# Kernel tuning notes

Measured on AMD Instinct MI355X. Metric: run time of the kernel, lower is better.

The kernel has to match this reference:

```python
import jax, jax.numpy as jnp
import numpy as np

B, T, OBS, H, LAT = 512, 512, 64, 256, 16
NEG_SLOPE = 0.01  # flax nn.leaky_relu default


def _glorot(key, shape):
    fan_in, fan_out = shape[0], shape[-1]
    s = jnp.sqrt(6.0 / (fan_in + fan_out))
    return jax.random.uniform(key, shape, jnp.float32, -s, s)


def setup_inputs() -> dict:
    key = jax.random.key(0)
    ks = jax.random.split(key, 12)
    x = jax.random.normal(ks[0], (B, T, OBS), jnp.float32)
    lengths = jax.random.randint(ks[1], (B,), T // 4, T + 1)
    mask = jnp.arange(T)[None, :] < lengths[:, None]  # [B,T] bool, prefix-valid
    return {
        "x": x,
        "mask": mask,
        # encoder params
        "Wip": _glorot(ks[2], (OBS, H)), "bip": jnp.zeros((H,)),
        "Wi_e": _glorot(ks[3], (H, 4 * H)), "Wh_e": _glorot(ks[4], (H, 4 * H)),
        "b_e": jnp.zeros((4 * H,)),
        "Wlp": _glorot(ks[5], (H, LAT)), "blp": jnp.zeros((LAT,)),
        # decoder params
        "Wle": _glorot(ks[6], (LAT, H)), "ble": jnp.zeros((H,)),
        "Wi_d": _glorot(ks[7], (H, 4 * H)), "Wh_d": _glorot(ks[8], (H, 4 * H)),
        "b_d": jnp.zeros((4 * H,)),
        "Wop": _glorot(ks[9], (H, OBS)), "bop": jnp.zeros((OBS,)),
    }


def _lstm_step(c, h, x_t, Wi, Wh, b):
    # flax OptimizedLSTMCell: fused gates, order i, f, g, o
    z = x_t @ Wi + h @ Wh + b  # [B, 4H]
    i, f, g, o = jnp.split(z, 4, axis=-1)
    new_c = jax.nn.sigmoid(f) * c + jax.nn.sigmoid(i) * jnp.tanh(g)
    new_h = jax.nn.sigmoid(o) * jnp.tanh(new_c)
    return new_c, new_h


def _forward(x, mask, Wip, bip, Wi_e, Wh_e, b_e, Wlp, blp,
             Wle, ble, Wi_d, Wh_d, b_d, Wop, bop):
    # ---- Encoder ----
    xp = jax.nn.leaky_relu(x @ Wip + bip, NEG_SLOPE)  # [B,T,H]
    xs = (jnp.swapaxes(xp, 0, 1), jnp.swapaxes(mask, 0, 1)[:, :, None])  # [T,B,H],[T,B,1]

    def enc_step(carry, inp):
        c, h = carry
        x_t, m_t = inp
        nc, nh = _lstm_step(c, h, x_t, Wi_e, Wh_e, b_e)
        # masked carry update (MaskedLSTMCell)
        return (jnp.where(m_t, nc, c), jnp.where(m_t, nh, h)), None

    init = (jnp.zeros((x.shape[0], Wh_e.shape[0]), x.dtype),
            jnp.zeros((x.shape[0], Wh_e.shape[0]), x.dtype))
    (c_f, h_f), _ = jax.lax.scan(enc_step, init, xs)
    latent = h_f @ Wlp + blp  # [B,LAT]

    ctx = jax.nn.leaky_relu(latent @ Wle + ble, NEG_SLOPE)  # [B,H]

    def dec_step(carry, _):
        c, h = carry
        nc, nh = _lstm_step(c, h, h, Wi_d, Wh_d, b_d)
        pred = nh @ Wop + bop
        return (nc, nh), pred

    _, recon = jax.lax.scan(dec_step, (ctx, ctx), None, length=T)  # [T,B,OBS]
    recon = jnp.swapaxes(recon, 0, 1)  # [B,T,OBS]
    return recon, latent


def reference(x, mask, Wip, bip, Wi_e, Wh_e, b_e, Wlp, blp,
              Wle, ble, Wi_d, Wh_d, b_d, Wop, bop):
    return _forward(x, mask, Wip, bip, Wi_e, Wh_e, b_e, Wlp, blp,
                    Wle, ble, Wi_d, Wh_d, b_d, Wop, bop)
```

## Files before the change

### kernel.cpp

```cpp
#include <hip/hip_runtime.h>

typedef unsigned short u16;
typedef unsigned u32;
typedef unsigned long long u64;
typedef float f32x4 __attribute__((ext_vector_type(4)));
typedef __bf16 bf16x8 __attribute__((ext_vector_type(8)));
typedef u32 u32x4 __attribute__((ext_vector_type(4)));

#define NT_ 512
#define LD 264
#define SPIN_GUARD 100000

__device__ __forceinline__ u16 f2bf(float f) {
  unsigned u = __builtin_bit_cast(unsigned, f);
  u += 0x7FFFu + ((u >> 16) & 1u);
  return (u16)(u >> 16);
}
__device__ __forceinline__ float bf2f(u16 h) {
  unsigned u = ((unsigned)h) << 16;
  return __builtin_bit_cast(float, u);
}
__device__ __forceinline__ f32x4 splat4(float b) { f32x4 v = {b, b, b, b}; return v; }
__device__ __forceinline__ bf16x8 asb(uint4 v) { return __builtin_bit_cast(bf16x8, v); }
__device__ __forceinline__ float sigf(float v) { return 1.0f / (1.0f + exp2f(-1.44269504f * v)); }
__device__ __forceinline__ float tanhf_(float v) { float e = exp2f(2.88539008f * v); return 1.0f - 2.0f / (e + 1.0f); }

__device__ __forceinline__ void barL() {
  asm volatile("s_waitcnt lgkmcnt(0)\n\ts_barrier" ::: "memory");
}

__device__ __forceinline__ void pub4(u32* p, u32x4 v) {
  asm volatile("global_store_dwordx4 %0, %1, off sc0 sc1" :: "v"(p), "v"(v) : "memory");
}

__device__ __forceinline__ void poll3(const u32* a0, const u32* a1, const u32* a2,
                                      u32 tg, u32x4& r0, u32x4& r1, u32x4& r2) {
  int gdn = 0;
  while (true) {
    u32x4 t0, t1, t2;
    asm volatile(
        "global_load_dwordx4 %0, %3, off sc0 sc1\n\t"
        "global_load_dwordx4 %1, %4, off sc0 sc1\n\t"
        "global_load_dwordx4 %2, %5, off sc0 sc1\n\t"
        "s_waitcnt vmcnt(0)"
        : "=&v"(t0), "=&v"(t1), "=&v"(t2)
        : "v"(a0), "v"(a1), "v"(a2)
        : "memory");
    bool ok = (t0[0] >> 16) == tg && (t0[1] >> 16) == tg &&
              (t0[2] >> 16) == tg && (t0[3] >> 16) == tg &&
              (t1[0] >> 16) == tg && (t1[1] >> 16) == tg &&
              (t1[2] >> 16) == tg && (t1[3] >> 16) == tg &&
              (t2[0] >> 16) == tg && (t2[1] >> 16) == tg &&
              (t2[2] >> 16) == tg && (t2[3] >> 16) == tg;
    if (ok || ++gdn >= SPIN_GUARD) { r0 = t0; r1 = t1; r2 = t2; return; }
  }
}

__global__ void k_pack_g(const float* __restrict__ src, const float* __restrict__ src2,
                         u16* __restrict__ dst) {
  int e = blockIdx.x * 256 + threadIdx.x;
  int j = e & 7, lane = (e >> 3) & 63, g = (e >> 9) & 3, ks = (e >> 11) & 7;
  int w = (e >> 14) & 3, s = (e >> 16) & 3;
  int k = ks * 32 + ((lane >> 4) << 3) + j;
  int col = g * 256 + s * 64 + w * 16 + (lane & 15);
  float v = src[k * 1024 + col];
  if (src2) v += src2[k * 1024 + col];
  dst[e] = f2bf(v);
}
__global__ void k_pack_wip(const float* __restrict__ Wip, u16* __restrict__ dst) {
  int e = blockIdx.x * 256 + threadIdx.x;
  int j = e & 7, lane = (e >> 3) & 63, n = (e >> 9) & 3, ks2 = (e >> 11) & 1, w = (e >> 12) & 3;
  int k = ks2 * 32 + ((lane >> 4) << 3) + j;
  int col = w * 64 + n * 16 + (lane & 15);
  dst[e] = f2bf(Wip[k * 256 + col]);
}
__global__ void k_pack_wop(const float* __restrict__ Wop, u16* __restrict__ dst) {
  int e = blockIdx.x * 256 + threadIdx.x;
  int j = e & 7, lane = (e >> 3) & 63, ks = (e >> 9) & 7, s = (e >> 12) & 3;
  int k = ks * 32 + ((lane >> 4) << 3) + j;
  int col = s * 16 + (lane & 15);
  dst[e] = f2bf(Wop[k * 64 + col]);
}

__global__ void k_lens(const unsigned char* __restrict__ mask, int* __restrict__ skeys) {
  int b = threadIdx.x;
  bool u8 = (mask[1] | mask[2] | mask[3]) != 0;
  int s = 0;
  if (u8) { const unsigned char* row = mask + b * NT_; for (int t = 0; t < NT_; t++) s += row[t] ? 1 : 0; }
  else { const int* row = (const int*)mask + b * NT_; for (int t = 0; t < NT_; t++) s += row[t] ? 1 : 0; }
  skeys[b] = s * 1024 + b;
}

__global__ void k_sort(int* __restrict__ skeys) {
  __shared__ int sk[512];
  int tid = threadIdx.x;
  sk[tid] = skeys[tid];
  __syncthreads();
  for (int k = 2; k <= 512; k <<= 1)
    for (int j = k >> 1; j > 0; j >>= 1) {
      int ixj = tid ^ j;
      if (ixj > tid) {
        int a = sk[tid], b = sk[ixj];
        bool up = ((tid & k) == 0);
        if ((a > b) == up) { sk[tid] = b; sk[ixj] = a; }
      }
      __syncthreads();
    }
  skeys[tid] = sk[tid];
}

__global__ void k_zero_hpub(u32* __restrict__ hp) {
  int i = blockIdx.x * 256 + threadIdx.x;
  u32x4 z = {0u, 0u, 0u, 0u};
  pub4(hp + (size_t)i * 4, z);
}

__global__ __launch_bounds__(256, 1) void k_rec4(
    const float* __restrict__ x,
    const u16* __restrict__ whe_p, const u16* __restrict__ wie_p,
    const u16* __restrict__ wd_p, const u16* __restrict__ wip_p,
    const u16* __restrict__ wop_p,
    const float* __restrict__ bip, const float* __restrict__ be,
    const float* __restrict__ Wlp, const float* __restrict__ blp,
    const float* __restrict__ Wle, const float* __restrict__ ble,
    const float* __restrict__ bd, const float* __restrict__ bop,
    const int* __restrict__ skeys,
    u32* __restrict__ hpub, float* __restrict__ out) {
  __shared__ __align__(16) u16 hx[16 * LD];
  __shared__ __align__(16) u16 xps[16 * LD];
  __shared__ __align__(16) u16 xbuf[16 * 72];
  __shared__ int ob_s[16], len_s[16];
  __shared__ float lat_s[256];

  const int tid = threadIdx.x;
  const int w = tid >> 6, lane = tid & 63, q = lane >> 4, n16 = lane & 15;
  const int b = blockIdx.x;
  const int g = (b & 7) + ((b >> 5) << 3);
  const int s = (b >> 3) & 3;

  if (tid < 16) {
    int v = skeys[g * 16 + tid];
    ob_s[tid] = v & 1023;
    len_s[tid] = v >> 10;
  }
  for (int i = tid; i < 16 * LD; i += 256) hx[i] = 0;
  __syncthreads();
  int maxlen = 0;
#pragma unroll
  for (int i = 0; i < 16; i++) maxlen = len_s[i] > maxlen ? len_s[i] : maxlen;
  int mylen[4];
#pragma unroll
  for (int r = 0; r < 4; r++) mylen[r] = len_s[q * 4 + r];

  const uint4* whe4 = (const uint4*)whe_p;
  const uint4* wie4 = (const uint4*)wie_p;
  const uint4* wip4 = (const uint4*)wip_p;
  uint4 wfh[32], wfx[32], wipf[8];
#pragma unroll
  for (int f = 0; f < 32; f++) wfh[f] = whe4[((s * 4 + w) * 32 + f) * 64 + lane];
#pragma unroll
  for (int f = 0; f < 32; f++) wfx[f] = wie4[((s * 4 + w) * 32 + f) * 64 + lane];
#pragma unroll
  for (int f = 0; f < 8; f++) wipf[f] = wip4[(w * 8 + f) * 64 + lane];

  float be_r[4], bipr[4];
#pragma unroll
  for (int gt = 0; gt < 4; gt++) be_r[gt] = be[gt * 256 + s * 64 + w * 16 + n16];
#pragma unroll
  for (int n = 0; n < 4; n++) bipr[n] = bip[w * 64 + n * 16 + n16];

  float creg[4], hreg[4];
#pragma unroll
  for (int r = 0; r < 4; r++) { creg[r] = 0.f; hreg[r] = 0.f; }

  const char* hxb = (const char*)hx;
  const char* xpsb = (const char*)xps;
  u32* hp32 = hpub + (size_t)g * 8192;
  const int p0 = (s == 0) ? 1 : 0;
  const int p1 = (s <= 1) ? 2 : 1;
  const int p2 = (s <= 2) ? 3 : 2;
  const int widx = ((tid >> 2) << 4) + ((tid & 3) << 2);
  const int ccl = tid >> 2, qq = tid & 3;
  const int cc0 = p0 * 64 + ccl, cc1 = p1 * 64 + ccl, cc2 = p2 * 64 + ccl;
  u32* pubp = hp32 + s * 1024 + ((w * 16 + n16) << 4) + (q << 2);
  const int mycol = s * 64 + w * 16 + n16;

#define SCAT3()                                  \
  do {                                           \
    hx[(qq * 4 + 0) * LD + cc0] = (u16)r0[0];    \
    hx[(qq * 4 + 1) * LD + cc0] = (u16)r0[1];    \
    hx[(qq * 4 + 2) * LD + cc0] = (u16)r0[2];    \
    hx[(qq * 4 + 3) * LD + cc0] = (u16)r0[3];    \
    hx[(qq * 4 + 0) * LD + cc1] = (u16)r1[0];    \
    hx[(qq * 4 + 1) * LD + cc1] = (u16)r1[1];    \
    hx[(qq * 4 + 2) * LD + cc1] = (u16)r1[2];    \
    hx[(qq * 4 + 3) * LD + cc1] = (u16)r1[3];    \
    hx[(qq * 4 + 0) * LD + cc2] = (u16)r2[0];    \
    hx[(qq * 4 + 1) * LD + cc2] = (u16)r2[1];    \
    hx[(qq * 4 + 2) * LD + cc2] = (u16)r2[2];    \
    hx[(qq * 4 + 3) * LD + cc2] = (u16)r2[3];    \
  } while (0)

  const float4* xr4 = (const float4*)x + (size_t)ob_s[tid >> 4] * 8192 + (tid & 15);
  float4 xv = xr4[0];

  for (int t = 0; t < maxlen; t++) {
    {
      u64 pv = (u64)f2bf(xv.x) | ((u64)f2bf(xv.y) << 16) |
               ((u64)f2bf(xv.z) << 32) | ((u64)f2bf(xv.w) << 48);
      *(u64*)&xbuf[(tid >> 4) * 72 + (tid & 15) * 4] = pv;
    }
    int tn = (t + 1 < maxlen) ? t + 1 : t;
    float4 xnx = xr4[(size_t)tn * 16];
    barL();
    f32x4 xacc[4];
#pragma unroll
    for (int n = 0; n < 4; n++) xacc[n] = splat4(bipr[n]);
#pragma unroll
    for (int ks2 = 0; ks2 < 2; ks2++) {
      bf16x8 a = *(const bf16x8*)((const char*)xbuf + n16 * 144 + ks2 * 64 + q * 16);
#pragma unroll
      for (int n = 0; n < 4; n++)
        xacc[n] = __builtin_amdgcn_mfma_f32_16x16x32_bf16(a, asb(wipf[ks2 * 4 + n]), xacc[n], 0, 0, 0);
    }
#pragma unroll
    for (int n = 0; n < 4; n++)
#pragma unroll
      for (int r = 0; r < 4; r++) {
        float v = xacc[n][r];
        v = v >= 0.f ? v : 0.01f * v;
        xps[(q * 4 + r) * LD + w * 64 + n * 16 + n16] = f2bf(v);
      }
    barL();
    f32x4 acc[4];
#pragma unroll
    for (int gt = 0; gt < 4; gt++) acc[gt] = splat4(be_r[gt]);
#pragma unroll
    for (int ks = 0; ks < 8; ks++) {
      bf16x8 a = *(const bf16x8*)(xpsb + n16 * (LD * 2) + ks * 64 + q * 16);
#pragma unroll
      for (int gt = 0; gt < 4; gt++)
        acc[gt] = __builtin_amdgcn_mfma_f32_16x16x32_bf16(a, asb(wfx[ks * 4 + gt]), acc[gt], 0, 0, 0);
    }
    if (t > 0) {
      const u32* bp = hp32 + ((t & 1) << 12);
      u32x4 r0, r1, r2;
      poll3(bp + p0 * 1024 + widx, bp + p1 * 1024 + widx, bp + p2 * 1024 + widx,
            (u32)t, r0, r1, r2);
      SCAT3();
    }
    barL();
#pragma unroll
    for (int ks = 0; ks < 8; ks++) {
      bf16x8 a = *(const bf16x8*)(hxb + n16 * (LD * 2) + ks * 64 + q * 16);
#pragma unroll
      for (int gt = 0; gt < 4; gt++)
        acc[gt] = __builtin_amdgcn_mfma_f32_16x16x32_bf16(a, asb(wfh[ks * 4 + gt]), acc[gt], 0, 0, 0);
    }
    u16 hb[4];
#pragma unroll
    for (int r = 0; r < 4; r++) {
      float i_ = sigf(acc[0][r]);
      float f_ = sigf(acc[1][r]);
      float g_ = tanhf_(acc[2][r]);
      float o_ = sigf(acc[3][r]);
      float nc = f_ * creg[r] + i_ * g_;
      float nh = o_ * tanhf_(nc);
      bool upd = t < mylen[r];
      creg[r] = upd ? nc : creg[r];
      hreg[r] = upd ? nh : hreg[r];
      hb[r] = f2bf(hreg[r]);
    }
    {
      u32 tgw = (u32)(t + 1) << 16;
      u32x4 pv = {tgw | hb[0], tgw | hb[1], tgw | hb[2], tgw | hb[3]};
      pub4(pubp + (((t + 1) & 1) << 12), pv);
    }
    barL();
#pragma unroll
    for (int r = 0; r < 4; r++) hx[(q * 4 + r) * LD + mycol] = hb[r];
    xv = xnx;
  }

  {
    const u32* bp = hp32 + ((maxlen & 1) << 12);
    u32x4 r0, r1, r2;
    poll3(bp + p0 * 1024 + widx, bp + p1 * 1024 + widx, bp + p2 * 1024 + widx,
          (u32)maxlen, r0, r1, r2);
    SCAT3();
  }
  barL();

  {
    int m = tid >> 4, j = tid & 15;
    float acc_ = blp[j];
    for (int k = 0; k < 256; k++) acc_ = fmaf(bf2f(hx[m * LD + k]), Wlp[k * 16 + j], acc_);
    if (s == 0) out[16777216 + ob_s[m] * 16 + j] = acc_;
    lat_s[m * 16 + j] = acc_;
  }
  __syncthreads();
  for (int i = tid; i < 4096; i += 256) {
    int m = i >> 8, c = i & 255;
    float v = ble[c];
#pragma unroll
    for (int k = 0; k < 16; k++) v = fmaf(lat_s[m * 16 + k], Wle[k * 256 + c], v);
    v = v >= 0.f ? v : 0.01f * v;
    hx[m * LD + c] = f2bf(v);
  }
  __syncthreads();
#pragma unroll
  for (int r = 0; r < 4; r++) {
    hreg[r] = bf2f(hx[(q * 4 + r) * LD + mycol]);
    creg[r] = hreg[r];
  }

  const uint4* wd4 = (const uint4*)wd_p;
  const uint4* wop4 = (const uint4*)wop_p;
#pragma unroll
  for (int f = 0; f < 32; f++) wfh[f] = wd4[((s * 4 + w) * 32 + f) * 64 + lane];
#pragma unroll
  for (int f = 0; f < 8; f++) wfx[f] = wop4[(s * 8 + f) * 64 + lane];
  float bd_r[4];
#pragma unroll
  for (int gt = 0; gt < 4; gt++) bd_r[gt] = bd[gt * 256 + s * 64 + w * 16 + n16];
  float bop_r = bop[s * 16 + n16];
  int orow[4];
#pragma unroll
  for (int r = 0; r < 4; r++) orow[r] = ob_s[q * 4 + r] << 15;
  const int E = maxlen;

  for (int d = 0; d < NT_; d++) {
    if (d > 0) {
      const u32* bp = hp32 + (((E + d) & 1) << 12);
      u32x4 r0, r1, r2;
      poll3(bp + p0 * 1024 + widx, bp + p1 * 1024 + widx, bp + p2 * 1024 + widx,
            (u32)(E + d), r0, r1, r2);
      SCAT3();
    }
    barL();
    f32x4 pacc = splat4(0.f);
#pragma unroll
    for (int ks = 0; ks < 8; ks++) {
      bf16x8 a = *(const bf16x8*)(hxb + n16 * (LD * 2) + ks * 64 + q * 16);
      pacc = __builtin_amdgcn_mfma_f32_16x16x32_bf16(a, asb(wfx[ks]), pacc, 0, 0, 0);
    }
    if (w == 0 && d > 0) {
#pragma unroll
      for (int r = 0; r < 4; r++)
        out[orow[r] + ((d - 1) << 6) + (s << 4) + n16] = pacc[r] + bop_r;
    }
    f32x4 acc[4];
#pragma unroll
    for (int gt = 0; gt < 4; gt++) acc[gt] = splat4(bd_r[gt]);
#pragma unroll
    for (int ks = 0; ks < 8; ks++) {
      bf16x8 a = *(const bf16x8*)(hxb + n16 * (LD * 2) + ks * 64 + q * 16);
#pragma unroll
      for (int gt = 0; gt < 4; gt++)
        acc[gt] = __builtin_amdgcn_mfma_f32_16x16x32_bf16(a, asb(wfh[ks * 4 + gt]), acc[gt], 0, 0, 0);
    }
    u16 hb[4];
#pragma unroll
    for (int r = 0; r < 4; r++) {
      float i_ = sigf(acc[0][r]);
      float f_ = sigf(acc[1][r]);
      float g_ = tanhf_(acc[2][r]);
      float o_ = sigf(acc[3][r]);
      float nc = f_ * creg[r] + i_ * g_;
      creg[r] = nc;
      hreg[r] = o_ * tanhf_(nc);
      hb[r] = f2bf(hreg[r]);
    }
    {
      u32 tgw = (u32)(E + d + 1) << 16;
      u32x4 pv = {tgw | hb[0], tgw | hb[1], tgw | hb[2], tgw | hb[3]};
      pub4(pubp + (((E + d + 1) & 1) << 12), pv);
    }
    barL();
#pragma unroll
    for (int r = 0; r < 4; r++) hx[(q * 4 + r) * LD + mycol] = hb[r];
  }
  {
    const u32* bp = hp32 + (((E + NT_) & 1) << 12);
    u32x4 r0, r1, r2;
    poll3(bp + p0 * 1024 + widx, bp + p1 * 1024 + widx, bp + p2 * 1024 + widx,
          (u32)(E + NT_), r0, r1, r2);
    SCAT3();
  }
  barL();
  if (w == 0) {
    f32x4 pacc = splat4(0.f);
#pragma unroll
    for (int ks = 0; ks < 8; ks++) {
      bf16x8 a = *(const bf16x8*)(hxb + n16 * (LD * 2) + ks * 64 + q * 16);
      pacc = __builtin_amdgcn_mfma_f32_16x16x32_bf16(a, asb(wfx[ks]), pacc, 0, 0, 0);
    }
#pragma unroll
    for (int r = 0; r < 4; r++)
      out[orow[r] + (511 << 6) + (s << 4) + n16] = pacc[r] + bop_r;
  }
#undef SCAT3
}

#define OFF_WHE 0ull
#define OFF_WIE 524288ull
#define OFF_WD 1048576ull
#define OFF_WIP 1572864ull
#define OFF_WOP 1605632ull
#define OFF_HPUB 1638400ull
#define OFF_SKEYS 2686976ull
#define MIN_WS 2689024ull

extern "C" void kernel_launch(void* const* d_in, const int* in_sizes, int n_in,
                              void* d_out, int out_size, void* d_ws, size_t ws_size,
                              hipStream_t stream) {
  const float* x = (const float*)d_in[0];
  const unsigned char* mask = (const unsigned char*)d_in[1];
  const float* Wip = (const float*)d_in[2];
  const float* bip = (const float*)d_in[3];
  const float* Wie = (const float*)d_in[4];
  const float* Whe = (const float*)d_in[5];
  const float* be = (const float*)d_in[6];
  const float* Wlp = (const float*)d_in[7];
  const float* blp = (const float*)d_in[8];
  const float* Wle = (const float*)d_in[9];
  const float* ble = (const float*)d_in[10];
  const float* Wid = (const float*)d_in[11];
  const float* Whd = (const float*)d_in[12];
  const float* bd = (const float*)d_in[13];
  const float* Wop = (const float*)d_in[14];
  const float* bop = (const float*)d_in[15];
  float* out = (float*)d_out;
  char* ws = (char*)d_ws;

  if (ws_size < MIN_WS) return;

  u16* whe_p = (u16*)(ws + OFF_WHE);
  u16* wie_p = (u16*)(ws + OFF_WIE);
  u16* wd_p = (u16*)(ws + OFF_WD);
  u16* wip_p = (u16*)(ws + OFF_WIP);
  u16* wop_p = (u16*)(ws + OFF_WOP);
  u32* hpub = (u32*)(ws + OFF_HPUB);
  int* skeys = (int*)(ws + OFF_SKEYS);

  k_pack_g<<<1024, 256, 0, stream>>>(Whe, nullptr, whe_p);
  k_pack_g<<<1024, 256, 0, stream>>>(Wie, nullptr, wie_p);
  k_pack_g<<<1024, 256, 0, stream>>>(Wid, Whd, wd_p);
  k_pack_wip<<<64, 256, 0, stream>>>(Wip, wip_p);
  k_pack_wop<<<64, 256, 0, stream>>>(Wop, wop_p);
  k_lens<<<1, 512, 0, stream>>>(mask, skeys);
  k_sort<<<1, 512, 0, stream>>>(skeys);
  k_zero_hpub<<<256, 256, 0, stream>>>(hpub);

  k_rec4<<<128, 256, 0, stream>>>(x, whe_p, wie_p, wd_p, wip_p, wop_p,
                                  bip, be, Wlp, blp, Wle, ble, bd, bop,
                                  skeys, hpub, out);
}
```

Before: 2.802 ms.

## Double-buffer hidden state and software-pipeline input projection off the recurrence critical path

Double-buffers the hx, xps and xbuf shared tiles so each step needs only one barrier instead of two or three. The input projection and x@Wi gate contribution for the next step are computed after publishing h, overlapping the cross-block wait. The decoder output projection is moved after the publish so it runs off the critical path. This costs more shared memory and register pressure, and adds more complex parity bookkeeping with a risk of hazards between buffers.

```diff
diff --git a/kernel.cpp b/kernel.cpp
--- a/kernel.cpp
+++ b/kernel.cpp
@@ -9,6 +9,7 @@
 
 #define NT_ 512
 #define LD 264
+#define HXN (16 * LD)
 #define SPIN_GUARD 100000
 
 __device__ __forceinline__ u16 f2bf(float f) {
@@ -115,7 +116,7 @@
   pub4(hp + (size_t)i * 4, z);
 }
 
-__global__ __launch_bounds__(256, 1) void k_rec4(
+__global__ __launch_bounds__(256, 1) void k_rec6(
     const float* __restrict__ x,
     const u16* __restrict__ whe_p, const u16* __restrict__ wie_p,
     const u16* __restrict__ wd_p, const u16* __restrict__ wip_p,
@@ -126,9 +127,9 @@
     const float* __restrict__ bd, const float* __restrict__ bop,
     const int* __restrict__ skeys,
     u32* __restrict__ hpub, float* __restrict__ out) {
-  __shared__ __align__(16) u16 hx[16 * LD];
-  __shared__ __align__(16) u16 xps[16 * LD];
-  __shared__ __align__(16) u16 xbuf[16 * 72];
+  __shared__ __align__(16) u16 hx[2 * HXN];
+  __shared__ __align__(16) u16 xps[2 * HXN];
+  __shared__ __align__(16) u16 xbuf[2 * 16 * 72];
   __shared__ int ob_s[16], len_s[16];
   __shared__ float lat_s[256];
 
@@ -143,7 +144,7 @@
     ob_s[tid] = v & 1023;
     len_s[tid] = v >> 10;
   }
-  for (int i = tid; i < 16 * LD; i += 256) hx[i] = 0;
+  for (int i = tid; i < 2 * HXN; i += 256) hx[i] = 0;
   __syncthreads();
   int maxlen = 0;
 #pragma unroll
@@ -172,6 +173,7 @@
   float creg[4], hreg[4];
 #pragma unroll
   for (int r = 0; r < 4; r++) { creg[r] = 0.f; hreg[r] = 0.f; }
+  u16 hb[4] = {0, 0, 0, 0};
 
   const char* hxb = (const char*)hx;
   const char* xpsb = (const char*)xps;
@@ -184,80 +186,101 @@
   const int cc0 = p0 * 64 + ccl, cc1 = p1 * 64 + ccl, cc2 = p2 * 64 + ccl;
   u32* pubp = hp32 + s * 1024 + ((w * 16 + n16) << 4) + (q << 2);
   const int mycol = s * 64 + w * 16 + n16;
-
-#define SCAT3()                                  \
-  do {                                           \
-    hx[(qq * 4 + 0) * LD + cc0] = (u16)r0[0];    \
-    hx[(qq * 4 + 1) * LD + cc0] = (u16)r0[1];    \
-    hx[(qq * 4 + 2) * LD + cc0] = (u16)r0[2];    \
-    hx[(qq * 4 + 3) * LD + cc0] = (u16)r0[3];    \
-    hx[(qq * 4 + 0) * LD + cc1] = (u16)r1[0];    \
-    hx[(qq * 4 + 1) * LD + cc1] = (u16)r1[1];    \
-    hx[(qq * 4 + 2) * LD + cc1] = (u16)r1[2];    \
-    hx[(qq * 4 + 3) * LD + cc1] = (u16)r1[3];    \
-    hx[(qq * 4 + 0) * LD + cc2] = (u16)r2[0];    \
-    hx[(qq * 4 + 1) * LD + cc2] = (u16)r2[1];    \
-    hx[(qq * 4 + 2) * LD + cc2] = (u16)r2[2];    \
-    hx[(qq * 4 + 3) * LD + cc2] = (u16)r2[3];    \
+  u32x4 T0 = {0, 0, 0, 0}, T1 = {0, 0, 0, 0}, T2 = {0, 0, 0, 0};
+
+#define SCAT3(DSTB)                                \
+  do {                                             \
+    u16* D_ = (DSTB);                              \
+    D_[(qq * 4 + 0) * LD + cc0] = (u16)T0[0];      \
+    D_[(qq * 4 + 1) * LD + cc0] = (u16)T0[1];      \
+    D_[(qq * 4 + 2) * LD + cc0] = (u16)T0[2];      \
+    D_[(qq * 4 + 3) * LD + cc0] = (u16)T0[3];      \
+    D_[(qq * 4 + 0) * LD + cc1] = (u16)T1[0];      \
+    D_[(qq * 4 + 1) * LD + cc1] = (u16)T1[1];      \
+    D_[(qq * 4 + 2) * LD + cc1] = (u16)T1[2];      \
+    D_[(qq * 4 + 3) * LD + cc1] = (u16)T1[3];      \
+    D_[(qq * 4 + 0) * LD + cc2] = (u16)T2[0];      \
+    D_[(qq * 4 + 1) * LD + cc2] = (u16)T2[1];      \
+    D_[(qq * 4 + 2) * LD + cc2] = (u16)T2[2];      \
+    D_[(qq * 4 + 3) * LD + cc2] = (u16)T2[3];      \
   } while (0)
 
+#define STAGEX(vv, par)                                                  \
+  do {                                                                   \
+    u64 pv_ = (u64)f2bf((vv).x) | ((u64)f2bf((vv).y) << 16) |            \
+              ((u64)f2bf((vv).z) << 32) | ((u64)f2bf((vv).w) << 48);     \
+    *(u64*)&xbuf[(par) * 1152 + (tid >> 4) * 72 + (tid & 15) * 4] = pv_; \
+  } while (0)
+
+#define XPCOMP(par)                                                                           \
+  do {                                                                                        \
+    f32x4 xacc_[4];                                                                           \
+    _Pragma("unroll") for (int n = 0; n < 4; n++) xacc_[n] = splat4(bipr[n]);                 \
+    _Pragma("unroll") for (int ks2 = 0; ks2 < 2; ks2++) {                                     \
+      bf16x8 a_ = *(const bf16x8*)((const char*)xbuf + (par) * 2304 + n16 * 144 +             \
+                                   ks2 * 64 + q * 16);                                        \
+      _Pragma("unroll") for (int n = 0; n < 4; n++)                                           \
+          xacc_[n] = __builtin_amdgcn_mfma_f32_16x16x32_bf16(a_, asb(wipf[ks2 * 4 + n]),      \
+                                                             xacc_[n], 0, 0, 0);              \
+    }                                                                                         \
+    _Pragma("unroll") for (int n = 0; n < 4; n++) _Pragma("unroll") for (int r = 0; r < 4;    \
+                                                                         r++) {               \
+      float v_ = xacc_[n][r];                                                                 \
+      v_ = v_ >= 0.f ? v_ : 0.01f * v_;                                                       \
+      xps[(par) * HXN + (q * 4 + r) * LD + w * 64 + n * 16 + n16] = f2bf(v_);                 \
+    }                                                                                         \
+  } while (0)
+
   const float4* xr4 = (const float4*)x + (size_t)ob_s[tid >> 4] * 8192 + (tid & 15);
-  float4 xv = xr4[0];
+
+  float4 xvA;
+  f32x4 z1acc[4];
+  {
+    float4 xv0 = xr4[0];
+    float4 xv1 = xr4[16];
+    xvA = xr4[32];
+    STAGEX(xv0, 0);
+    __syncthreads();
+    XPCOMP(0);
+    STAGEX(xv1, 1);
+    __syncthreads();
+    XPCOMP(1);
+    __syncthreads();
+#pragma unroll
+    for (int gt = 0; gt < 4; gt++) z1acc[gt] = splat4(be_r[gt]);
+#pragma unroll
+    for (int ks = 0; ks < 8; ks++) {
+      bf16x8 a = *(const bf16x8*)(xpsb + n16 * (LD * 2) + ks * 64 + q * 16);
+#pragma unroll
+      for (int gt = 0; gt < 4; gt++)
+        z1acc[gt] = __builtin_amdgcn_mfma_f32_16x16x32_bf16(a, asb(wfx[ks * 4 + gt]), z1acc[gt], 0, 0, 0);
+    }
+  }
 
   for (int t = 0; t < maxlen; t++) {
-    {
-      u64 pv = (u64)f2bf(xv.x) | ((u64)f2bf(xv.y) << 16) |
-               ((u64)f2bf(xv.z) << 32) | ((u64)f2bf(xv.w) << 48);
-      *(u64*)&xbuf[(tid >> 4) * 72 + (tid & 15) * 4] = pv;
-    }
-    int tn = (t + 1 < maxlen) ? t + 1 : t;
-    float4 xnx = xr4[(size_t)tn * 16];
-    barL();
-    f32x4 xacc[4];
-#pragma unroll
-    for (int n = 0; n < 4; n++) xacc[n] = splat4(bipr[n]);
-#pragma unroll
-    for (int ks2 = 0; ks2 < 2; ks2++) {
-      bf16x8 a = *(const bf16x8*)((const char*)xbuf + n16 * 144 + ks2 * 64 + q * 16);
-#pragma unroll
-      for (int n = 0; n < 4; n++)
-        xacc[n] = __builtin_amdgcn_mfma_f32_16x16x32_bf16(a, asb(wipf[ks2 * 4 + n]), xacc[n], 0, 0, 0);
-    }
-#pragma unroll
-    for (int n = 0; n < 4; n++)
-#pragma unroll
-      for (int r = 0; r < 4; r++) {
-        float v = xacc[n][r];
-        v = v >= 0.f ? v : 0.01f * v;
-        xps[(q * 4 + r) * LD + w * 64 + n * 16 + n16] = f2bf(v);
-      }
+    const int par = t & 1;
+    const u32* bp = hp32 + (par << 12);
+    const u32* pa0 = bp + p0 * 1024 + widx;
+    const u32* pa1 = bp + p1 * 1024 + widx;
+    const u32* pa2 = bp + p2 * 1024 + widx;
+    STAGEX(xvA, par);
+#pragma unroll
+    for (int r = 0; r < 4; r++) hx[par * HXN + (q * 4 + r) * LD + mycol] = hb[r];
+    if (t > 0) {
+      poll3(pa0, pa1, pa2, (u32)t, T0, T1, T2);
+      SCAT3(hx + par * HXN);
+    }
     barL();
     f32x4 acc[4];
 #pragma unroll
-    for (int gt = 0; gt < 4; gt++) acc[gt] = splat4(be_r[gt]);
+    for (int gt = 0; gt < 4; gt++) acc[gt] = z1acc[gt];
 #pragma unroll
     for (int ks = 0; ks < 8; ks++) {
-      bf16x8 a = *(const bf16x8*)(xpsb + n16 * (LD * 2) + ks * 64 + q * 16);
-#pragma unroll
-      for (int gt = 0; gt < 4; gt++)
-        acc[gt] = __builtin_amdgcn_mfma_f32_16x16x32_bf16(a, asb(wfx[ks * 4 + gt]), acc[gt], 0, 0, 0);
-    }
-    if (t > 0) {
-      const u32* bp = hp32 + ((t & 1) << 12);
-      u32x4 r0, r1, r2;
-      poll3(bp + p0 * 1024 + widx, bp + p1 * 1024 + widx, bp + p2 * 1024 + widx,
-            (u32)t, r0, r1, r2);
-      SCAT3();
-    }
-    barL();
-#pragma unroll
-    for (int ks = 0; ks < 8; ks++) {
-      bf16x8 a = *(const bf16x8*)(hxb + n16 * (LD * 2) + ks * 64 + q * 16);
+      bf16x8 a = *(const bf16x8*)(hxb + par * (HXN * 2) + n16 * (LD * 2) + ks * 64 + q * 16);
 #pragma unroll
       for (int gt = 0; gt < 4; gt++)
         acc[gt] = __builtin_amdgcn_mfma_f32_16x16x32_bf16(a, asb(wfh[ks * 4 + gt]), acc[gt], 0, 0, 0);
     }
-    u16 hb[4];
 #pragma unroll
     for (int r = 0; r < 4; r++) {
       float i_ = sigf(acc[0][r]);
@@ -276,25 +299,41 @@
       u32x4 pv = {tgw | hb[0], tgw | hb[1], tgw | hb[2], tgw | hb[3]};
       pub4(pubp + (((t + 1) & 1) << 12), pv);
     }
+    int tl = t + 3;
+    tl = tl < maxlen ? tl : maxlen - 1;
+    float4 xnx = xr4[(size_t)tl * 16];
+#pragma unroll
+    for (int gt = 0; gt < 4; gt++) z1acc[gt] = splat4(be_r[gt]);
+#pragma unroll
+    for (int ks = 0; ks < 8; ks++) {
+      bf16x8 a = *(const bf16x8*)(xpsb + (par ^ 1) * (HXN * 2) + n16 * (LD * 2) + ks * 64 + q * 16);
+#pragma unroll
+      for (int gt = 0; gt < 4; gt++)
+        z1acc[gt] = __builtin_amdgcn_mfma_f32_16x16x32_bf16(a, asb(wfx[ks * 4 + gt]), z1acc[gt], 0, 0, 0);
+    }
+    XPCOMP(par);
+    xvA = xnx;
+  }
+
+  {
+    const int par = maxlen & 1;
+    const u32* bp = hp32 + (par << 12);
+    const u32* pa0 = bp + p0 * 1024 + widx;
+    const u32* pa1 = bp + p1 * 1024 + widx;
+    const u32* pa2 = bp + p2 * 1024 + widx;
+#pragma unroll
+    for (int r = 0; r < 4; r++) hx[par * HXN + (q * 4 + r) * LD + mycol] = hb[r];
+    poll3(pa0, pa1, pa2, (u32)maxlen, T0, T1, T2);
+    SCAT3(hx + par * HXN);
     barL();
-#pragma unroll
-    for (int r = 0; r < 4; r++) hx[(q * 4 + r) * LD + mycol] = hb[r];
-    xv = xnx;
   }
 
   {
-    const u32* bp = hp32 + ((maxlen & 1) << 12);
-    u32x4 r0, r1, r2;
-    poll3(bp + p0 * 1024 + widx, bp + p1 * 1024 + widx, bp + p2 * 1024 + widx,
-          (u32)maxlen, r0, r1, r2);
-    SCAT3();
-  }
-  barL();
-
-  {
+    const int hpar = maxlen & 1;
     int m = tid >> 4, j = tid & 15;
     float acc_ = blp[j];
-    for (int k = 0; k < 256; k++) acc_ = fmaf(bf2f(hx[m * LD + k]), Wlp[k * 16 + j], acc_);
+    for (int k = 0; k < 256; k++)
+      acc_ = fmaf(bf2f(hx[hpar * HXN + m * LD + k]), Wlp[k * 16 + j], acc_);
     if (s == 0) out[16777216 + ob_s[m] * 16 + j] = acc_;
     lat_s[m * 16 + j] = acc_;
   }
@@ -312,6 +351,7 @@
   for (int r = 0; r < 4; r++) {
     hreg[r] = bf2f(hx[(q * 4 + r) * LD + mycol]);
     creg[r] = hreg[r];
+    hb[r] = f2bf(hreg[r]);
   }
 
   const uint4* wd4 = (const uint4*)wd_p;
@@ -330,36 +370,28 @@
   const int E = maxlen;
 
   for (int d = 0; d < NT_; d++) {
+    const int par = d & 1;
+    const u32* bp = hp32 + (((E + d) & 1) << 12);
+    const u32* pa0 = bp + p0 * 1024 + widx;
+    const u32* pa1 = bp + p1 * 1024 + widx;
+    const u32* pa2 = bp + p2 * 1024 + widx;
     if (d > 0) {
-      const u32* bp = hp32 + (((E + d) & 1) << 12);
-      u32x4 r0, r1, r2;
-      poll3(bp + p0 * 1024 + widx, bp + p1 * 1024 + widx, bp + p2 * 1024 + widx,
-            (u32)(E + d), r0, r1, r2);
-      SCAT3();
+#pragma unroll
+      for (int r = 0; r < 4; r++) hx[par * HXN + (q * 4 + r) * LD + mycol] = hb[r];
+      poll3(pa0, pa1, pa2, (u32)(E + d), T0, T1, T2);
+      SCAT3(hx + par * HXN);
     }
     barL();
-    f32x4 pacc = splat4(0.f);
+    f32x4 acc[4];
+#pragma unroll
+    for (int gt = 0; gt < 4; gt++) acc[gt] = splat4(bd_r[gt]);
 #pragma unroll
     for (int ks = 0; ks < 8; ks++) {
-      bf16x8 a = *(const bf16x8*)(hxb + n16 * (LD * 2) + ks * 64 + q * 16);
-      pacc = __builtin_amdgcn_mfma_f32_16x16x32_bf16(a, asb(wfx[ks]), pacc, 0, 0, 0);
-    }
-    if (w == 0 && d > 0) {
-#pragma unroll
-      for (int r = 0; r < 4; r++)
-        out[orow[r] + ((d - 1) << 6) + (s << 4) + n16] = pacc[r] + bop_r;
-    }
-    f32x4 acc[4];
-#pragma unroll
-    for (int gt = 0; gt < 4; gt++) acc[gt] = splat4(bd_r[gt]);
-#pragma unroll
-    for (int ks = 0; ks < 8; ks++) {
-      bf16x8 a = *(const bf16x8*)(hxb + n16 * (LD * 2) + ks * 64 + q * 16);
+      bf16x8 a = *(const bf16x8*)(hxb + par * (HXN * 2) + n16 * (LD * 2) + ks * 64 + q * 16);
 #pragma unroll
       for (int gt = 0; gt < 4; gt++)
         acc[gt] = __builtin_amdgcn_mfma_f32_16x16x32_bf16(a, asb(wfh[ks * 4 + gt]), acc[gt], 0, 0, 0);
     }
-    u16 hb[4];
 #pragma unroll
     for (int r = 0; r < 4; r++) {
       float i_ = sigf(acc[0][r]);
@@ -376,30 +408,44 @@
       u32x4 pv = {tgw | hb[0], tgw | hb[1], tgw | hb[2], tgw | hb[3]};
       pub4(pubp + (((E + d + 1) & 1) << 12), pv);
     }
-    barL();
-#pragma unroll
-    for (int r = 0; r < 4; r++) hx[(q * 4 + r) * LD + mycol] = hb[r];
-  }
+    if (w == 0 && d >= 1) {
+      f32x4 pacc = splat4(0.f);
+#pragma unroll
+      for (int ks = 0; ks < 8; ks++) {
+        bf16x8 a = *(const bf16x8*)(hxb + par * (HXN * 2) + n16 * (LD * 2) + ks * 64 + q * 16);
+        pacc = __builtin_amdgcn_mfma_f32_16x16x32_bf16(a, asb(wfx[ks]), pacc, 0, 0, 0);
+      }
+#pragma unroll
+      for (int r = 0; r < 4; r++)
+        out[orow[r] + ((d - 1) << 6) + (s << 4) + n16] = pacc[r] + bop_r;
+    }
+  }
+
   {
     const u32* bp = hp32 + (((E + NT_) & 1) << 12);
-    u32x4 r0, r1, r2;
-    poll3(bp + p0 * 1024 + widx, bp + p1 * 1024 + widx, bp + p2 * 1024 + widx,
-          (u32)(E + NT_), r0, r1, r2);
-    SCAT3();
-  }
-  barL();
-  if (w == 0) {
-    f32x4 pacc = splat4(0.f);
-#pragma unroll
-    for (int ks = 0; ks < 8; ks++) {
-      bf16x8 a = *(const bf16x8*)(hxb + n16 * (LD * 2) + ks * 64 + q * 16);
-      pacc = __builtin_amdgcn_mfma_f32_16x16x32_bf16(a, asb(wfx[ks]), pacc, 0, 0, 0);
-    }
-#pragma unroll
-    for (int r = 0; r < 4; r++)
-      out[orow[r] + (511 << 6) + (s << 4) + n16] = pacc[r] + bop_r;
+    const u32* pa0 = bp + p0 * 1024 + widx;
+    const u32* pa1 = bp + p1 * 1024 + widx;
+    const u32* pa2 = bp + p2 * 1024 + widx;
+#pragma unroll
+    for (int r = 0; r < 4; r++) hx[(q * 4 + r) * LD + mycol] = hb[r];
+    poll3(pa0, pa1, pa2, (u32)(E + NT_), T0, T1, T2);
+    SCAT3(hx);
+    barL();
+    if (w == 0) {
+      f32x4 pacc = splat4(0.f);
+#pragma unroll
+      for (int ks = 0; ks < 8; ks++) {
+        bf16x8 a = *(const bf16x8*)(hxb + n16 * (LD * 2) + ks * 64 + q * 16);
+        pacc = __builtin_amdgcn_mfma_f32_16x16x32_bf16(a, asb(wfx[ks]), pacc, 0, 0, 0);
+      }
+#pragma unroll
+      for (int r = 0; r < 4; r++)
+        out[orow[r] + (511 << 6) + (s << 4) + n16] = pacc[r] + bop_r;
+    }
   }
 #undef SCAT3
+#undef STAGEX
+#undef XPCOMP
 }
 
 #define OFF_WHE 0ull
@@ -452,7 +498,7 @@
   k_sort<<<1, 512, 0, stream>>>(skeys);
   k_zero_hpub<<<256, 256, 0, stream>>>(hpub);
 
-  k_rec4<<<128, 256, 0, stream>>>(x, whe_p, wie_p, wd_p, wip_p, wop_p,
+  k_rec6<<<128, 256, 0, stream>>>(x, whe_p, wie_p, wd_p, wip_p, wop_p,
                                   bip, be, Wlp, blp, Wle, ble, bd, bop,
                                   skeys, hpub, out);
 }
```

Result: no change. 2.812 ms (+0.4%).
